# Kernel tuning notes

Measured on AMD Instinct MI355X. Metric: run time of the kernel, lower is better.

The kernel has to match this reference:

```python
import jax, jax.numpy as jnp
import numpy as np

# dims
N, E, Z, C, NB = 8192, 131072, 10, 128, 8
R_MAX, P_CUT, AVG_NEIGH = 5.0, 5, 16.0
SH_DIM, N_L, N_LAYERS, MLP_H = 16, 4, 2, 16
# which l each of the 16 sh components belongs to
L_OF_M = jnp.array([0, 1, 1, 1, 2, 2, 2, 2, 2, 3, 3, 3, 3, 3, 3, 3])


def spherical_harmonics(u):
    """Real spherical harmonics up to l=3, e3nn 'component' normalization. u: [E,3] unit vectors."""
    x, y, z = u[:, 0], u[:, 1], u[:, 2]
    x2, y2, z2 = x * x, y * y, z * z
    s3, s5, s15 = np.sqrt(3.0), np.sqrt(5.0), np.sqrt(15.0)
    a33, a32, a31, a30 = 0.25 * np.sqrt(70.0), np.sqrt(105.0), 0.25 * np.sqrt(42.0), 0.5 * np.sqrt(7.0)
    Y = [jnp.ones_like(x),
         s3 * x, s3 * y, s3 * z,
         s15 * x * y, s15 * y * z, 0.5 * s5 * (3 * z2 - 1.0), s15 * x * z, 0.5 * s15 * (x2 - y2),
         a33 * y * (3 * x2 - y2), a32 * x * y * z, a31 * y * (5 * z2 - 1.0),
         a30 * z * (5 * z2 - 3.0), a31 * x * (5 * z2 - 1.0), 0.5 * a32 * z * (x2 - y2),
         a33 * x * (x2 - 3 * y2)]
    return jnp.stack(Y, axis=-1)  # [E,16]


def radial_embedding(r):
    """Bessel radial basis with smooth polynomial cutoff (p=5). r: [E] edge lengths."""
    x = r / R_MAX
    p = float(P_CUT)
    cut = (1.0 - 0.5 * (p + 1.0) * (p + 2.0) * x ** P_CUT
           + p * (p + 2.0) * x ** (P_CUT + 1) - 0.5 * p * (p + 1.0) * x ** (P_CUT + 2))
    cut = jnp.where(x < 1.0, cut, 0.0)
    n = jnp.arange(1, NB + 1, dtype=r.dtype)
    bessel = np.sqrt(2.0 / R_MAX) * jnp.sin(n[None, :] * jnp.pi * x[:, None]) / r[:, None]
    return bessel * cut[:, None]  # [E,8]


def _forward(positions, node_attrs, shifts, W_embed, W_up, R_w1, R_w2, R_w3,
             W_out, w_sc, w_prod, W_plin, w_ro0, ro_w1, ro_w2, edge_index):
    sender, receiver = edge_index[0], edge_index[1]
    vec = positions[receiver] - positions[sender] + shifts          # [E,3]
    lengths = jnp.linalg.norm(vec, axis=-1) + 1e-9                  # [E]
    sh = spherical_harmonics(vec / lengths[:, None])                # [E,16]
    edge_feats = radial_embedding(lengths)                          # [E,8]

    # node embedding: scalars into l=0 slot of [N,C,16]
    scalars = node_attrs @ W_embed                                  # [N,C]
    feats = jnp.zeros((N, C, SH_DIM), scalars.dtype).at[:, :, 0].set(scalars)

    outputs = []
    for L in range(N_LAYERS):
        # linear up (channel mixing, per irrep component)
        h = jnp.einsum('ncm,cd->ndm', feats, W_up[L])               # [N,C,16]
        # radial MLP -> per-edge, per-channel, per-l tensor-product weights
        r = jax.nn.silu(edge_feats @ R_w1[L])
        r = jax.nn.silu(r @ R_w2[L])
        w = (r @ R_w3[L]).reshape(E, C, N_L)                        # [E,C,4]
        w_m = jnp.take(w, L_OF_M, axis=2)                           # [E,C,16]
        # channel-wise tensor product: scalar node feat x SH, scatter to receiver
        msg = h[sender, :, 0][:, :, None] * w_m * sh[:, None, :]    # [E,C,16]
        agg = jax.ops.segment_sum(msg, receiver, num_segments=N) / AVG_NEIGH
        m = jnp.einsum('ncm,cd->ndm', agg, W_out[L])                # [N,C,16]
        # element-dependent skip connection
        sc = h * (node_attrs @ w_sc[L])[:, :, None]
        # product basis (correlation 3): element-weighted powers of scalar part
        s = m[:, :, 0]                                              # [N,C]
        coeff = jnp.einsum('nz,zck->nck', node_attrs, w_prod[L])    # [N,C,3]
        powers = jnp.stack([jnp.ones_like(s), s, s * s], axis=-1)   # [N,C,3]
        scale = jnp.sum(coeff * powers, axis=-1)                    # [N,C]
        feats = jnp.einsum('ncm,cd->ndm', m * scale[:, :, None], W_plin[L]) + sc
        if L == 0:
            outputs.append(feats[:, :, 0] @ w_ro0)                  # linear readout [N]
        else:
            outputs.append(jax.nn.silu(feats[:, :, 0] @ ro_w1) @ ro_w2)  # nonlinear readout [N]
    return outputs[0] + outputs[1]


def setup_inputs() -> dict:
    key = jax.random.key(0)
    ks = jax.random.split(key, 16)
    positions = jax.random.normal(ks[0], (N, 3), jnp.float32) * 1.5
    elems = jax.random.randint(ks[1], (N,), 0, Z)
    node_attrs = jax.nn.one_hot(elems, Z, dtype=jnp.float32)
    edge_index = jax.random.randint(ks[2], (2, E), 0, N)
    shifts = jnp.zeros((E, 3), jnp.float32)
    g = lambda k, sh, fan: jax.random.normal(k, sh, jnp.float32) / np.sqrt(fan)
    return {
        'positions': positions, 'node_attrs': node_attrs, 'shifts': shifts,
        'W_embed': g(ks[3], (Z, C), Z),
        'W_up': g(ks[4], (N_LAYERS, C, C), C),
        'R_w1': g(ks[5], (N_LAYERS, NB, 64), NB),
        'R_w2': g(ks[6], (N_LAYERS, 64, 64), 64),
        'R_w3': g(ks[7], (N_LAYERS, 64, C * N_L), 64),
        'W_out': g(ks[8], (N_LAYERS, C, C), C),
        'w_sc': g(ks[9], (N_LAYERS, Z, C), 1),
        'w_prod': g(ks[10], (N_LAYERS, Z, C, 3), 1) * 0.1,
        'W_plin': g(ks[11], (N_LAYERS, C, C), C),
        'w_ro0': g(ks[12], (C,), C),
        'ro_w1': g(ks[13], (C, MLP_H), C),
        'ro_w2': g(ks[14], (MLP_H,), MLP_H),
        'edge_index': edge_index,
    }


def reference(positions, node_attrs, shifts, W_embed, W_up, R_w1, R_w2, R_w3,
              W_out, w_sc, w_prod, W_plin, w_ro0, ro_w1, ro_w2, edge_index):
    return _forward(positions, node_attrs, shifts, W_embed, W_up, R_w1, R_w2, R_w3,
                    W_out, w_sc, w_prod, W_plin, w_ro0, ro_w1, ro_w2, edge_index)
```

## Files before the change

kernel.cpp:

```cpp
#include <hip/hip_runtime.h>
#include <math.h>

constexpr int kN = 8192;
constexpr int kE = 131072;
constexpr int kHalfN = 4096;
constexpr int kWbTiles = 544;
constexpr int kWbRows  = kWbTiles * 128;

typedef short bf16x8 __attribute__((ext_vector_type(8)));
typedef float f32x4 __attribute__((ext_vector_type(4)));
typedef unsigned short ushort_t;
typedef unsigned int uint_t;

__device__ __forceinline__ float silu_f(float x) { return x / (1.f + __expf(-x)); }

__device__ __forceinline__ ushort_t f2b(float f) {
  uint_t x = __float_as_uint(f);
  uint_t r = (x + 0x7fffu + ((x >> 16) & 1u)) >> 16;
  return (ushort_t)r;
}
__device__ __forceinline__ float b2f(ushort_t u) {
  return __uint_as_float(((uint_t)u) << 16);
}

__global__ __launch_bounds__(256) void zero_ints_kernel(int* __restrict__ a, int* __restrict__ b) {
  int i = blockIdx.x * 256 + threadIdx.x;
  if (i < kN) { a[i] = 0; b[i] = 0; }
}

__global__ __launch_bounds__(256) void elem_kernel(const float* __restrict__ attrs, int* __restrict__ elem) {
  int n = blockIdx.x * 256 + threadIdx.x;
  if (n >= kN) return;
  const float* a = attrs + (size_t)n * 10;
  int best = 0; float bv = a[0];
  #pragma unroll
  for (int z = 1; z < 10; ++z) { float v = a[z]; if (v > bv) { bv = v; best = z; } }
  elem[n] = best;
}

__global__ __launch_bounds__(256) void init_feats_kernel(const float* __restrict__ W_embed,
                                                         const int* __restrict__ elem,
                                                         ushort_t* __restrict__ F) {
  int i = blockIdx.x * 256 + threadIdx.x;
  int n = i >> 7, c = i & 127;
  F[(size_t)n * 2048 + c] = f2b(W_embed[(size_t)elem[n] * 128 + c]);
}

__global__ __launch_bounds__(256) void geom_kernel(const float* __restrict__ pos,
                                                   const float* __restrict__ shifts,
                                                   const int* __restrict__ ei,
                                                   float* __restrict__ sh,
                                                   float* __restrict__ rb) {
  int e = blockIdx.x * 256 + threadIdx.x;
  if (e >= kE) return;
  int s = ei[e], r = ei[kE + e];
  float vx = pos[r*3+0] - pos[s*3+0] + shifts[(size_t)e*3+0];
  float vy = pos[r*3+1] - pos[s*3+1] + shifts[(size_t)e*3+1];
  float vz = pos[r*3+2] - pos[s*3+2] + shifts[(size_t)e*3+2];
  float len = sqrtf(vx*vx + vy*vy + vz*vz) + 1e-9f;
  float inv = 1.f / len;
  float x = vx*inv, y = vy*inv, z = vz*inv;
  float x2 = x*x, y2 = y*y, z2 = z*z;
  const float s3  = 1.7320508075688772f;
  const float s5  = 2.2360679774997896f;
  const float s15 = 3.8729833462074170f;
  const float a33 = 2.0916500663351889f;
  const float a32 = 10.246950765959598f;
  const float a31 = 1.6201851746019651f;
  const float a30 = 1.3228756555322954f;
  float4* shp = (float4*)(sh + (size_t)e * 16);
  shp[0] = make_float4(1.f, s3*x, s3*y, s3*z);
  shp[1] = make_float4(s15*x*y, s15*y*z, 0.5f*s5*(3.f*z2 - 1.f), s15*x*z);
  shp[2] = make_float4(0.5f*s15*(x2 - y2), a33*y*(3.f*x2 - y2), a32*x*y*z, a31*y*(5.f*z2 - 1.f));
  shp[3] = make_float4(a30*z*(5.f*z2 - 3.f), a31*x*(5.f*z2 - 1.f), 0.5f*a32*z*(x2 - y2), a33*x*(x2 - 3.f*y2));
  float xr = len * 0.2f;
  float cut = 0.f;
  if (xr < 1.f) {
    float x5 = xr*xr*xr*xr*xr;
    cut = 1.f - 21.f*x5 + 35.f*x5*xr - 15.f*x5*xr*xr;
  }
  float pref = 0.63245553203367587f * cut * inv;
  const float PI = 3.14159265358979323846f;
  float theta = PI * xr;
  float sn, cs;
  __sincosf(theta, &sn, &cs);
  float twoc = 2.f * cs;
  float b[8];
  float s_prev = 0.f, s_cur = sn;
  b[0] = pref * s_cur;
  #pragma unroll
  for (int k = 1; k < 8; ++k) {
    float s_next = twoc * s_cur - s_prev;
    s_prev = s_cur; s_cur = s_next;
    b[k] = pref * s_cur;
  }
  float4* rbp = (float4*)(rb + (size_t)e * 8);
  rbp[0] = make_float4(b[0], b[1], b[2], b[3]);
  rbp[1] = make_float4(b[4], b[5], b[6], b[7]);
}

__global__ __launch_bounds__(256) void count_kernel(const int* __restrict__ ei, int* __restrict__ counts) {
  int e = blockIdx.x * 256 + threadIdx.x;
  if (e < kE) atomicAdd(&counts[ei[kE + e]], 1);
}

__global__ __launch_bounds__(1024) void scan_kernel(const int* __restrict__ counts, int* __restrict__ offs) {
  __shared__ int tmp[1024];
  int t = threadIdx.x;
  int loc[8]; int s = 0;
  #pragma unroll
  for (int i = 0; i < 8; ++i) { loc[i] = s; s += counts[t*8 + i]; }
  tmp[t] = s;
  __syncthreads();
  for (int d = 1; d < 1024; d <<= 1) {
    int v = (t >= d) ? tmp[t - d] : 0;
    __syncthreads();
    tmp[t] += v;
    __syncthreads();
  }
  int pre = (t == 0) ? 0 : tmp[t - 1];
  #pragma unroll
  for (int i = 0; i < 8; ++i) offs[t*8 + i] = pre + loc[i];
  if (t == 1023) offs[kN] = tmp[1023];
}

__global__ __launch_bounds__(256) void fill_kernel(const int* __restrict__ ei, const int* __restrict__ offs,
                                                   int* __restrict__ cursor, int* __restrict__ eids) {
  int e = blockIdx.x * 256 + threadIdx.x;
  if (e >= kE) return;
  int r = ei[kE + e];
  int pos = atomicAdd(&cursor[r], 1);
  eids[offs[r] + pos] = e;
}

__global__ __launch_bounds__(256) void radial_kernel(const float* __restrict__ rb,
                                                     const float* __restrict__ W1,
                                                     const float* __restrict__ W2,
                                                     ushort_t* __restrict__ r2) {
  __shared__ float rbs[128][8];
  __shared__ float W1s[8*64];
  __shared__ ushort_t B2s[64][72];
  __shared__ ushort_t r1s[128][72];
  const int tid = threadIdx.x;
  const size_t ebase = (size_t)blockIdx.x * 128;
  {
    int r = tid >> 1, q = tid & 1;
    *(float4*)&rbs[r][q*4] = *(const float4*)&rb[(ebase + r)*8 + q*4];
  }
  for (int i = tid; i < 512; i += 256) W1s[i] = W1[i];
  for (int i = tid; i < 4096; i += 256) {
    int k = i >> 6, col = i & 63;
    B2s[col][k] = f2b(W2[i]);
  }
  __syncthreads();
  {
    int col = tid & 63;
    int r0 = (tid >> 6) * 32;
    #pragma unroll 4
    for (int rr = 0; rr < 32; ++rr) {
      int row = r0 + rr;
      float v = 0.f;
      #pragma unroll
      for (int i = 0; i < 8; ++i) v = fmaf(rbs[row][i], W1s[i*64 + col], v);
      r1s[row][col] = f2b(silu_f(v));
    }
  }
  __syncthreads();
  const int lane = tid & 63, wv = tid >> 6;
  const int wr = wv * 32;
  const int fr = lane & 15, kg = (lane >> 4) * 8;
  f32x4 acc[2][4] = {};
  #pragma unroll
  for (int ks = 0; ks < 2; ++ks) {
    const int k0 = ks*32 + kg;
    bf16x8 af[2], bfr[4];
    #pragma unroll
    for (int i = 0; i < 2; ++i) af[i] = *(const bf16x8*)&r1s[wr + i*16 + fr][k0];
    #pragma unroll
    for (int j = 0; j < 4; ++j) bfr[j] = *(const bf16x8*)&B2s[j*16 + fr][k0];
    #pragma unroll
    for (int i = 0; i < 2; ++i)
      #pragma unroll
      for (int j = 0; j < 4; ++j)
        acc[i][j] = __builtin_amdgcn_mfma_f32_16x16x32_bf16(af[i], bfr[j], acc[i][j], 0, 0, 0);
  }
  __syncthreads();
  const int dcol = lane & 15, drow4 = (lane >> 4) * 4;
  #pragma unroll
  for (int i = 0; i < 2; ++i)
    #pragma unroll
    for (int j = 0; j < 4; ++j)
      #pragma unroll
      for (int r = 0; r < 4; ++r) {
        int row = wr + i*16 + drow4 + r;
        int col = j*16 + dcol;
        r1s[row][col] = f2b(silu_f(acc[i][j][r]));
      }
  __syncthreads();
  for (int idx = tid * 8; idx < 128*64; idx += 256*8) {
    int r = idx >> 6, k = idx & 63;
    *(int4*)&r2[(ebase + r)*64 + k] = *(const int4*)&r1s[r][k];
  }
}

__global__ __launch_bounds__(256) void transpose_w_kernel(const float* __restrict__ W, ushort_t* __restrict__ WT) {
  int i = blockIdx.x * 256 + threadIdx.x;
  int d = i >> 7, c = i & 127;
  WT[i] = f2b(W[c*128 + d]);
}

__global__ __launch_bounds__(256) void transpose_r3_kernel(const float* __restrict__ R3, ushort_t* __restrict__ R3T) {
  int i = blockIdx.x * 256 + threadIdx.x;
  int t = i >> 6, j = i & 63;
  R3T[i] = f2b(R3[j*512 + t]);
}

template<bool SCALED, bool EPI, bool L0>
__global__ __launch_bounds__(256) void mgemm_kernel(
    const ushort_t* __restrict__ A, size_t aStride,
    const ushort_t* __restrict__ BT,
    ushort_t* __restrict__ O, size_t oStride,
    const float* __restrict__ scaleBuf,
    const ushort_t* __restrict__ Hbuf,
    const float* __restrict__ wscL,
    const int* __restrict__ elem)
{
  __shared__ ushort_t As[128][136];
  __shared__ ushort_t Bs[128][136];
  const int tid = threadIdx.x;
  const size_t rowbase = (size_t)blockIdx.x * 128;

  for (int idx = tid * 8; idx < 128 * 128; idx += 256 * 8) {
    int r = idx >> 7, k = idx & 127;
    *(int4*)&Bs[r][k] = *(const int4*)&BT[(size_t)r * 128 + k];
  }
  for (int idx = tid * 8; idx < 128 * 128; idx += 256 * 8) {
    int r = idx >> 7, k = idx & 127;
    size_t grow = rowbase + r;
    const ushort_t* ap = A + grow * aStride + k;
    if (SCALED) {
      const float* sp = scaleBuf + (grow >> 4) * 128 + k;
      uint_t u[4];
      #pragma unroll
      for (int q = 0; q < 4; ++q) {
        ushort_t lo = f2b(b2f(ap[2*q])   * sp[2*q]);
        ushort_t hi = f2b(b2f(ap[2*q+1]) * sp[2*q+1]);
        u[q] = (uint_t)lo | ((uint_t)hi << 16);
      }
      *(int4*)&As[r][k] = make_int4((int)u[0], (int)u[1], (int)u[2], (int)u[3]);
    } else {
      *(int4*)&As[r][k] = *(const int4*)ap;
    }
  }
  __syncthreads();

  const int lane = tid & 63, wv = tid >> 6;
  const int wr = (wv >> 1) * 64, wc = (wv & 1) * 64;
  const int fr = lane & 15;
  const int kg = (lane >> 4) * 8;
  f32x4 acc[4][4] = {};
  #pragma unroll
  for (int ks = 0; ks < 4; ++ks) {
    const int k0 = ks * 32 + kg;
    bf16x8 af[4], bfr[4];
    #pragma unroll
    for (int i = 0; i < 4; ++i) af[i]  = *(const bf16x8*)&As[wr + i*16 + fr][k0];
    #pragma unroll
    for (int j = 0; j < 4; ++j) bfr[j] = *(const bf16x8*)&Bs[wc + j*16 + fr][k0];
    #pragma unroll
    for (int i = 0; i < 4; ++i)
      #pragma unroll
      for (int j = 0; j < 4; ++j)
        acc[i][j] = __builtin_amdgcn_mfma_f32_16x16x32_bf16(af[i], bfr[j], acc[i][j], 0, 0, 0);
  }

  const int dcol = lane & 15, drow4 = (lane >> 4) * 4;
  #pragma unroll
  for (int i = 0; i < 4; ++i) {
    #pragma unroll
    for (int j = 0; j < 4; ++j) {
      int col = wc + j*16 + dcol;
      #pragma unroll
      for (int r = 0; r < 4; ++r) {
        int row = wr + i*16 + drow4 + r;
        size_t grow = rowbase + row;
        float v = acc[i][j][r];
        if (EPI) {
          if (!L0 || ((grow & 15) == 0)) {
            int ee = elem[grow >> 4];
            v += b2f(Hbuf[grow * 128 + col]) * wscL[(size_t)ee * 128 + col];
          }
        }
        O[grow * oStride + col] = f2b(v);
      }
    }
  }
}

__global__ __launch_bounds__(256) void wgemm_kernel(
    const ushort_t* __restrict__ r2, const int* __restrict__ eids,
    const int* __restrict__ offs, int nb0,
    const ushort_t* __restrict__ R3T, ushort_t* __restrict__ wb)
{
  __shared__ ushort_t As[128][72];
  __shared__ ushort_t Bs[128][72];
  const int tid = threadIdx.x;
  const int rowbase = blockIdx.x * 128;
  const int colbase = blockIdx.y * 128;
  const int halfStart = offs[nb0];
  const int halfEnd   = offs[nb0 + kHalfN];

  for (int idx = tid * 8; idx < 128 * 64; idx += 256 * 8) {
    int r = idx >> 6, k = idx & 63;
    *(int4*)&Bs[r][k] = *(const int4*)&R3T[(size_t)(colbase + r) * 64 + k];
  }
  for (int idx = tid * 8; idx < 128 * 64; idx += 256 * 8) {
    int r = idx >> 6, k = idx & 63;
    int ii = halfStart + rowbase + r;
    int iic = ii < halfEnd ? ii : (halfEnd - 1);
    if (iic < 0) iic = 0;
    int e = eids[iic];
    *(int4*)&As[r][k] = *(const int4*)&r2[(size_t)e * 64 + k];
  }
  __syncthreads();

  const int lane = tid & 63, wv = tid >> 6;
  const int wr = (wv >> 1) * 64, wc = (wv & 1) * 64;
  const int fr = lane & 15;
  const int kg = (lane >> 4) * 8;
  f32x4 acc[4][4] = {};
  #pragma unroll
  for (int ks = 0; ks < 2; ++ks) {
    const int k0 = ks * 32 + kg;
    bf16x8 af[4], bfr[4];
    #pragma unroll
    for (int i = 0; i < 4; ++i) af[i]  = *(const bf16x8*)&As[wr + i*16 + fr][k0];
    #pragma unroll
    for (int j = 0; j < 4; ++j) bfr[j] = *(const bf16x8*)&Bs[wc + j*16 + fr][k0];
    #pragma unroll
    for (int i = 0; i < 4; ++i)
      #pragma unroll
      for (int j = 0; j < 4; ++j)
        acc[i][j] = __builtin_amdgcn_mfma_f32_16x16x32_bf16(af[i], bfr[j], acc[i][j], 0, 0, 0);
  }

  const int dcol = lane & 15, drow4 = (lane >> 4) * 4;
  #pragma unroll
  for (int i = 0; i < 4; ++i) {
    #pragma unroll
    for (int j = 0; j < 4; ++j) {
      int col = colbase + wc + j*16 + dcol;
      #pragma unroll
      for (int r = 0; r < 4; ++r) {
        int row = rowbase + wr + i*16 + drow4 + r;
        wb[(size_t)row * 512 + col] = f2b(acc[i][j][r]);
      }
    }
  }
}

constexpr int CH = 16;
__global__ __launch_bounds__(512) void gather_kernel(
    const int* __restrict__ offs, const int* __restrict__ eids,
    const int* __restrict__ ei, int nb0,
    const ushort_t* __restrict__ wb,
    const float* __restrict__ sh,
    const ushort_t* __restrict__ H,
    ushort_t* __restrict__ AGG)
{
  __shared__ ushort_t ws[CH][512];
  __shared__ ushort_t h0s[CH][128];
  __shared__ float shs[CH][16];
  int n = nb0 + blockIdx.x;
  int t = threadIdx.x;
  int l = t >> 7;
  int c = t & 127;
  const int wstart = offs[nb0];
  float a0=0,a1=0,a2=0,a3=0,a4=0,a5=0,a6=0;
  const int e0 = offs[n], e1 = offs[n+1];
  for (int base = e0; base < e1; base += CH) {
    const int cnt = min(CH, e1 - base);
    #pragma unroll
    for (int rep = 0; rep < 2; ++rep) {
      int idx = rep * 512 + t;
      int j = idx >> 6, seg = idx & 63;
      if (j < cnt)
        *(int4*)&ws[j][seg * 8] = *(const int4*)&wb[(size_t)(base - wstart + j) * 512 + seg * 8];
    }
    if (t < 256) {
      int j = t >> 4, seg = t & 15;
      if (j < cnt) {
        int e = eids[base + j];
        *(int4*)&h0s[j][seg * 8] = *(const int4*)&H[(size_t)ei[e] * 2048 + seg * 8];
      }
    } else if (t < 320) {
      int tt = t - 256, j = tt >> 2, seg = tt & 3;
      if (j < cnt)
        *(float4*)&shs[j][seg * 4] = *(const float4*)&sh[(size_t)eids[base + j] * 16 + seg * 4];
    }
    __syncthreads();
    for (int j = 0; j < cnt; ++j) {
      float wv = b2f(ws[j][(c << 2) | l]);
      float wh = wv * b2f(h0s[j][c]);
      if (l == 0) {
        a0 = fmaf(wh, shs[j][0], a0);
      } else if (l == 1) {
        float4 s4 = *(const float4*)&shs[j][0];
        a0 = fmaf(wh, s4.y, a0); a1 = fmaf(wh, s4.z, a1); a2 = fmaf(wh, s4.w, a2);
      } else if (l == 2) {
        float4 s4 = *(const float4*)&shs[j][4];
        float s8 = shs[j][8];
        a0 = fmaf(wh, s4.x, a0); a1 = fmaf(wh, s4.y, a1); a2 = fmaf(wh, s4.z, a2);
        a3 = fmaf(wh, s4.w, a3); a4 = fmaf(wh, s8, a4);
      } else {
        float4 sA = *(const float4*)&shs[j][8];
        float4 sB = *(const float4*)&shs[j][12];
        a0 = fmaf(wh, sA.y, a0); a1 = fmaf(wh, sA.z, a1); a2 = fmaf(wh, sA.w, a2);
        a3 = fmaf(wh, sB.x, a3); a4 = fmaf(wh, sB.y, a4); a5 = fmaf(wh, sB.z, a5);
        a6 = fmaf(wh, sB.w, a6);
      }
    }
    __syncthreads();
  }
  const float inv16 = 0.0625f;
  size_t baseo = (size_t)n * 2048 + c;
  if (l == 0) {
    AGG[baseo] = f2b(a0 * inv16);
  } else if (l == 1) {
    AGG[baseo + 1*128] = f2b(a0*inv16); AGG[baseo + 2*128] = f2b(a1*inv16); AGG[baseo + 3*128] = f2b(a2*inv16);
  } else if (l == 2) {
    AGG[baseo + 4*128] = f2b(a0*inv16); AGG[baseo + 5*128] = f2b(a1*inv16); AGG[baseo + 6*128] = f2b(a2*inv16);
    AGG[baseo + 7*128] = f2b(a3*inv16); AGG[baseo + 8*128] = f2b(a4*inv16);
  } else {
    AGG[baseo + 9*128]  = f2b(a0*inv16); AGG[baseo + 10*128] = f2b(a1*inv16); AGG[baseo + 11*128] = f2b(a2*inv16);
    AGG[baseo + 12*128] = f2b(a3*inv16); AGG[baseo + 13*128] = f2b(a4*inv16); AGG[baseo + 14*128] = f2b(a5*inv16);
    AGG[baseo + 15*128] = f2b(a6*inv16);
  }
}

__global__ __launch_bounds__(256) void scale_kernel(const ushort_t* __restrict__ M,
                                                    const int* __restrict__ elem,
                                                    const float* __restrict__ wprodL,
                                                    float* __restrict__ scale) {
  int i = blockIdx.x * 256 + threadIdx.x;
  int n = i >> 7, c = i & 127;
  float s = b2f(M[(size_t)n * 2048 + c]);
  const float* co = wprodL + ((size_t)elem[n] * 128 + c) * 3;
  scale[i] = co[0] + s * (co[1] + s * co[2]);
}

__global__ __launch_bounds__(64) void readout_kernel(const ushort_t* __restrict__ F,
                                                     const float* __restrict__ ro0,
                                                     const float* __restrict__ ro1,
                                                     const float* __restrict__ ro2,
                                                     float* __restrict__ out, int layer) {
  int n = blockIdx.x; int t = threadIdx.x;
  const ushort_t* fr = F + (size_t)n * 2048;
  float f0 = b2f(fr[t]), f1 = b2f(fr[t + 64]);
  if (layer == 0) {
    float v = f0 * ro0[t] + f1 * ro0[t + 64];
    #pragma unroll
    for (int m = 32; m > 0; m >>= 1) v += __shfl_xor(v, m, 64);
    if (t == 0) out[n] = v;
  } else {
    float acc = 0.f;
    for (int h = 0; h < 16; ++h) {
      float p = f0 * ro1[t*16 + h] + f1 * ro1[(t + 64)*16 + h];
      #pragma unroll
      for (int m = 32; m > 0; m >>= 1) p += __shfl_xor(p, m, 64);
      acc = fmaf(silu_f(p), ro2[h], acc);
    }
    if (t == 0) out[n] += acc;
  }
}

extern "C" void kernel_launch(void* const* d_in, const int* in_sizes, int n_in,
                              void* d_out, int out_size, void* d_ws, size_t ws_size,
                              hipStream_t stream) {
  (void)in_sizes; (void)n_in; (void)out_size;
  const float* positions = (const float*)d_in[0];
  const float* node_attrs= (const float*)d_in[1];
  const float* shifts    = (const float*)d_in[2];
  const float* W_embed   = (const float*)d_in[3];
  const float* W_up      = (const float*)d_in[4];
  const float* R_w1      = (const float*)d_in[5];
  const float* R_w2      = (const float*)d_in[6];
  const float* R_w3      = (const float*)d_in[7];
  const float* W_out     = (const float*)d_in[8];
  const float* w_sc      = (const float*)d_in[9];
  const float* w_prod    = (const float*)d_in[10];
  const float* W_plin    = (const float*)d_in[11];
  const float* w_ro0     = (const float*)d_in[12];
  const float* ro_w1     = (const float*)d_in[13];
  const float* ro_w2     = (const float*)d_in[14];
  const int*   ei        = (const int*)d_in[15];
  float* out = (float*)d_out;

  char* ws_ptr = (char*)d_ws;
  size_t off = 0;
  auto alloc = [&](size_t nbytes) -> void* {
    void* p = ws_ptr + off;
    off += (nbytes + 255) & ~(size_t)255;
    return p;
  };
  const size_t PB = (size_t)kN * 16 * 128 * sizeof(ushort_t);
  ushort_t* P0   = (ushort_t*)alloc(PB);
  ushort_t* P1   = (ushort_t*)alloc(PB);
  ushort_t* P2   = (ushort_t*)alloc(PB);
  float* shb     = (float*)alloc((size_t)kE * 16 * 4);
  float* rbb     = (float*)alloc((size_t)kE * 8 * 4);
  ushort_t* r2b  = (ushort_t*)alloc((size_t)kE * 64 * 2);
  float* scaleb  = (float*)alloc((size_t)kN * 128 * 4);
  ushort_t* wb   = (ushort_t*)alloc((size_t)kWbRows * 512 * 2);
  ushort_t* R3T0 = (ushort_t*)alloc(512 * 64 * 2);
  ushort_t* R3T1 = (ushort_t*)alloc(512 * 64 * 2);
  ushort_t* WTu0 = (ushort_t*)alloc(128 * 128 * 2);
  ushort_t* WTu1 = (ushort_t*)alloc(128 * 128 * 2);
  ushort_t* WTo0 = (ushort_t*)alloc(128 * 128 * 2);
  ushort_t* WTo1 = (ushort_t*)alloc(128 * 128 * 2);
  ushort_t* WTp0 = (ushort_t*)alloc(128 * 128 * 2);
  ushort_t* WTp1 = (ushort_t*)alloc(128 * 128 * 2);
  int* elemb  = (int*)alloc(kN * 4);
  int* counts = (int*)alloc(kN * 4);
  int* cursor = (int*)alloc(kN * 4);
  int* offsb  = (int*)alloc((kN + 1) * 4);
  int* eidsb  = (int*)alloc((size_t)kE * 4);
  if (off > ws_size) return;

  zero_ints_kernel<<<kN/256, 256, 0, stream>>>(counts, cursor);
  elem_kernel<<<kN/256, 256, 0, stream>>>(node_attrs, elemb);
  init_feats_kernel<<<(kN*128)/256, 256, 0, stream>>>(W_embed, elemb, P0);
  geom_kernel<<<kE/256, 256, 0, stream>>>(positions, shifts, ei, shb, rbb);
  count_kernel<<<kE/256, 256, 0, stream>>>(ei, counts);
  scan_kernel<<<1, 1024, 0, stream>>>(counts, offsb);
  fill_kernel<<<kE/256, 256, 0, stream>>>(ei, offsb, cursor, eidsb);
  transpose_w_kernel<<<64, 256, 0, stream>>>(W_up, WTu0);
  transpose_w_kernel<<<64, 256, 0, stream>>>(W_up + 16384, WTu1);
  transpose_w_kernel<<<64, 256, 0, stream>>>(W_out, WTo0);
  transpose_w_kernel<<<64, 256, 0, stream>>>(W_out + 16384, WTo1);
  transpose_w_kernel<<<64, 256, 0, stream>>>(W_plin, WTp0);
  transpose_w_kernel<<<64, 256, 0, stream>>>(W_plin + 16384, WTp1);
  transpose_r3_kernel<<<128, 256, 0, stream>>>(R_w3, R3T0);
  transpose_r3_kernel<<<128, 256, 0, stream>>>(R_w3 + 32768, R3T1);

  radial_kernel<<<kE/128, 256, 0, stream>>>(rbb, R_w1, R_w2, r2b);
  mgemm_kernel<false,false,false><<<kN/128, 256, 0, stream>>>(
      P0, 2048, WTu0, P1, 2048, nullptr, nullptr, nullptr, nullptr);
  wgemm_kernel<<<dim3(kWbTiles,4), 256, 0, stream>>>(r2b, eidsb, offsb, 0, R3T0, wb);
  gather_kernel<<<kHalfN, 512, 0, stream>>>(offsb, eidsb, ei, 0, wb, shb, P1, P2);
  wgemm_kernel<<<dim3(kWbTiles,4), 256, 0, stream>>>(r2b, eidsb, offsb, kHalfN, R3T0, wb);
  gather_kernel<<<kHalfN, 512, 0, stream>>>(offsb, eidsb, ei, kHalfN, wb, shb, P1, P2);
  mgemm_kernel<false,false,false><<<(kN*16)/128, 256, 0, stream>>>(
      P2, 128, WTo0, P0, 128, nullptr, nullptr, nullptr, nullptr);
  scale_kernel<<<(kN*128)/256, 256, 0, stream>>>(P0, elemb, w_prod, scaleb);
  mgemm_kernel<true,true,true><<<(kN*16)/128, 256, 0, stream>>>(
      P0, 128, WTp0, P2, 128, scaleb, P1, w_sc, elemb);
  readout_kernel<<<kN, 64, 0, stream>>>(P2, w_ro0, ro_w1, ro_w2, out, 0);

  radial_kernel<<<kE/128, 256, 0, stream>>>(rbb, R_w1 + 512, R_w2 + 4096, r2b);
  mgemm_kernel<false,false,false><<<(kN*16)/128, 256, 0, stream>>>(
      P2, 128, WTu1, P1, 128, nullptr, nullptr, nullptr, nullptr);
  wgemm_kernel<<<dim3(kWbTiles,4), 256, 0, stream>>>(r2b, eidsb, offsb, 0, R3T1, wb);
  gather_kernel<<<kHalfN, 512, 0, stream>>>(offsb, eidsb, ei, 0, wb, shb, P1, P0);
  wgemm_kernel<<<dim3(kWbTiles,4), 256, 0, stream>>>(r2b, eidsb, offsb, kHalfN, R3T1, wb);
  gather_kernel<<<kHalfN, 512, 0, stream>>>(offsb, eidsb, ei, kHalfN, wb, shb, P1, P0);
  mgemm_kernel<false,false,false><<<(kN*16)/128, 256, 0, stream>>>(
      P0, 128, WTo1, P2, 128, nullptr, nullptr, nullptr, nullptr);
  scale_kernel<<<(kN*128)/256, 256, 0, stream>>>(P2, elemb, w_prod + 3840, scaleb);
  mgemm_kernel<true,true,false><<<(kN*16)/128, 256, 0, stream>>>(
      P2, 128, WTp1, P0, 128, scaleb, P1, w_sc + 1280, elemb);
  readout_kernel<<<kN, 64, 0, stream>>>(P0, w_ro0, ro_w1, ro_w2, out, 1);
}
```

Baseline: 471.1 us.

## Fuse per-edge R3 weight GEMM into gather and store edge data in CSR order

Measured after the change: 662.1 us. 40.5% more time.

```diff
diff --git a/kernel.cpp b/kernel.cpp
--- a/kernel.cpp
+++ b/kernel.cpp
@@ -3,9 +3,6 @@
 
 constexpr int kN = 8192;
 constexpr int kE = 131072;
-constexpr int kHalfN = 4096;
-constexpr int kWbTiles = 544;
-constexpr int kWbRows  = kWbTiles * 128;
 
 typedef short bf16x8 __attribute__((ext_vector_type(8)));
 typedef float f32x4 __attribute__((ext_vector_type(4)));
@@ -46,14 +43,55 @@
   F[(size_t)n * 2048 + c] = f2b(W_embed[(size_t)elem[n] * 128 + c]);
 }
 
+__global__ __launch_bounds__(256) void count_kernel(const int* __restrict__ ei, int* __restrict__ counts) {
+  int e = blockIdx.x * 256 + threadIdx.x;
+  if (e < kE) atomicAdd(&counts[ei[kE + e]], 1);
+}
+
+__global__ __launch_bounds__(1024) void scan_kernel(const int* __restrict__ counts, int* __restrict__ offs) {
+  __shared__ int tmp[1024];
+  int t = threadIdx.x;
+  int loc[8]; int s = 0;
+  #pragma unroll
+  for (int i = 0; i < 8; ++i) { loc[i] = s; s += counts[t*8 + i]; }
+  tmp[t] = s;
+  __syncthreads();
+  for (int d = 1; d < 1024; d <<= 1) {
+    int v = (t >= d) ? tmp[t - d] : 0;
+    __syncthreads();
+    tmp[t] += v;
+    __syncthreads();
+  }
+  int pre = (t == 0) ? 0 : tmp[t - 1];
+  #pragma unroll
+  for (int i = 0; i < 8; ++i) offs[t*8 + i] = pre + loc[i];
+  if (t == 1023) offs[kN] = tmp[1023];
+}
+
+__global__ __launch_bounds__(256) void fill_kernel(const int* __restrict__ ei, const int* __restrict__ offs,
+                                                   int* __restrict__ cursor, int* __restrict__ eids,
+                                                   int* __restrict__ sends) {
+  int e = blockIdx.x * 256 + threadIdx.x;
+  if (e >= kE) return;
+  int s = ei[e];
+  int r = ei[kE + e];
+  int pos = atomicAdd(&cursor[r], 1);
+  eids[offs[r] + pos] = e;
+  sends[offs[r] + pos] = s;
+}
+
 __global__ __launch_bounds__(256) void geom_kernel(const float* __restrict__ pos,
                                                    const float* __restrict__ shifts,
                                                    const int* __restrict__ ei,
+                                                   const int* __restrict__ eids,
+                                                   const int* __restrict__ sends,
                                                    float* __restrict__ sh,
                                                    float* __restrict__ rb) {
-  int e = blockIdx.x * 256 + threadIdx.x;
-  if (e >= kE) return;
-  int s = ei[e], r = ei[kE + e];
+  int slot = blockIdx.x * 256 + threadIdx.x;
+  if (slot >= kE) return;
+  int e = eids[slot];
+  int s = sends[slot];
+  int r = ei[kE + e];
   float vx = pos[r*3+0] - pos[s*3+0] + shifts[(size_t)e*3+0];
   float vy = pos[r*3+1] - pos[s*3+1] + shifts[(size_t)e*3+1];
   float vz = pos[r*3+2] - pos[s*3+2] + shifts[(size_t)e*3+2];
@@ -68,7 +106,7 @@
   const float a32 = 10.246950765959598f;
   const float a31 = 1.6201851746019651f;
   const float a30 = 1.3228756555322954f;
-  float4* shp = (float4*)(sh + (size_t)e * 16);
+  float4* shp = (float4*)(sh + (size_t)slot * 16);
   shp[0] = make_float4(1.f, s3*x, s3*y, s3*z);
   shp[1] = make_float4(s15*x*y, s15*y*z, 0.5f*s5*(3.f*z2 - 1.f), s15*x*z);
   shp[2] = make_float4(0.5f*s15*(x2 - y2), a33*y*(3.f*x2 - y2), a32*x*y*z, a31*y*(5.f*z2 - 1.f));
@@ -94,43 +132,9 @@
     s_prev = s_cur; s_cur = s_next;
     b[k] = pref * s_cur;
   }
-  float4* rbp = (float4*)(rb + (size_t)e * 8);
+  float4* rbp = (float4*)(rb + (size_t)slot * 8);
   rbp[0] = make_float4(b[0], b[1], b[2], b[3]);
   rbp[1] = make_float4(b[4], b[5], b[6], b[7]);
-}
-
-__global__ __launch_bounds__(256) void count_kernel(const int* __restrict__ ei, int* __restrict__ counts) {
-  int e = blockIdx.x * 256 + threadIdx.x;
-  if (e < kE) atomicAdd(&counts[ei[kE + e]], 1);
-}
-
-__global__ __launch_bounds__(1024) void scan_kernel(const int* __restrict__ counts, int* __restrict__ offs) {
-  __shared__ int tmp[1024];
-  int t = threadIdx.x;
-  int loc[8]; int s = 0;
-  #pragma unroll
-  for (int i = 0; i < 8; ++i) { loc[i] = s; s += counts[t*8 + i]; }
-  tmp[t] = s;
-  __syncthreads();
-  for (int d = 1; d < 1024; d <<= 1) {
-    int v = (t >= d) ? tmp[t - d] : 0;
-    __syncthreads();
-    tmp[t] += v;
-    __syncthreads();
-  }
-  int pre = (t == 0) ? 0 : tmp[t - 1];
-  #pragma unroll
-  for (int i = 0; i < 8; ++i) offs[t*8 + i] = pre + loc[i];
-  if (t == 1023) offs[kN] = tmp[1023];
-}
-
-__global__ __launch_bounds__(256) void fill_kernel(const int* __restrict__ ei, const int* __restrict__ offs,
-                                                   int* __restrict__ cursor, int* __restrict__ eids) {
-  int e = blockIdx.x * 256 + threadIdx.x;
-  if (e >= kE) return;
-  int r = ei[kE + e];
-  int pos = atomicAdd(&cursor[r], 1);
-  eids[offs[r] + pos] = e;
 }
 
 __global__ __launch_bounds__(256) void radial_kernel(const float* __restrict__ rb,
@@ -212,7 +216,8 @@
 __global__ __launch_bounds__(256) void transpose_r3_kernel(const float* __restrict__ R3, ushort_t* __restrict__ R3T) {
   int i = blockIdx.x * 256 + threadIdx.x;
   int t = i >> 6, j = i & 63;
-  R3T[i] = f2b(R3[j*512 + t]);
+  int c = t & 127, l = t >> 7;
+  R3T[i] = f2b(R3[j*512 + c*4 + l]);
 }
 
 template<bool SCALED, bool EPI, bool L0>
@@ -297,144 +302,92 @@
   }
 }
 
-__global__ __launch_bounds__(256) void wgemm_kernel(
-    const ushort_t* __restrict__ r2, const int* __restrict__ eids,
-    const int* __restrict__ offs, int nb0,
-    const ushort_t* __restrict__ R3T, ushort_t* __restrict__ wb)
-{
-  __shared__ ushort_t As[128][72];
-  __shared__ ushort_t Bs[128][72];
-  const int tid = threadIdx.x;
-  const int rowbase = blockIdx.x * 128;
-  const int colbase = blockIdx.y * 128;
-  const int halfStart = offs[nb0];
-  const int halfEnd   = offs[nb0 + kHalfN];
-
-  for (int idx = tid * 8; idx < 128 * 64; idx += 256 * 8) {
-    int r = idx >> 6, k = idx & 63;
-    *(int4*)&Bs[r][k] = *(const int4*)&R3T[(size_t)(colbase + r) * 64 + k];
-  }
-  for (int idx = tid * 8; idx < 128 * 64; idx += 256 * 8) {
-    int r = idx >> 6, k = idx & 63;
-    int ii = halfStart + rowbase + r;
-    int iic = ii < halfEnd ? ii : (halfEnd - 1);
-    if (iic < 0) iic = 0;
-    int e = eids[iic];
-    *(int4*)&As[r][k] = *(const int4*)&r2[(size_t)e * 64 + k];
-  }
-  __syncthreads();
-
-  const int lane = tid & 63, wv = tid >> 6;
-  const int wr = (wv >> 1) * 64, wc = (wv & 1) * 64;
-  const int fr = lane & 15;
-  const int kg = (lane >> 4) * 8;
-  f32x4 acc[4][4] = {};
-  #pragma unroll
-  for (int ks = 0; ks < 2; ++ks) {
-    const int k0 = ks * 32 + kg;
-    bf16x8 af[4], bfr[4];
-    #pragma unroll
-    for (int i = 0; i < 4; ++i) af[i]  = *(const bf16x8*)&As[wr + i*16 + fr][k0];
-    #pragma unroll
-    for (int j = 0; j < 4; ++j) bfr[j] = *(const bf16x8*)&Bs[wc + j*16 + fr][k0];
-    #pragma unroll
-    for (int i = 0; i < 4; ++i)
-      #pragma unroll
-      for (int j = 0; j < 4; ++j)
-        acc[i][j] = __builtin_amdgcn_mfma_f32_16x16x32_bf16(af[i], bfr[j], acc[i][j], 0, 0, 0);
-  }
-
-  const int dcol = lane & 15, drow4 = (lane >> 4) * 4;
-  #pragma unroll
-  for (int i = 0; i < 4; ++i) {
-    #pragma unroll
-    for (int j = 0; j < 4; ++j) {
-      int col = colbase + wc + j*16 + dcol;
-      #pragma unroll
-      for (int r = 0; r < 4; ++r) {
-        int row = rowbase + wr + i*16 + drow4 + r;
-        wb[(size_t)row * 512 + col] = f2b(acc[i][j][r]);
-      }
-    }
-  }
-}
-
-constexpr int CH = 16;
 __global__ __launch_bounds__(512) void gather_kernel(
-    const int* __restrict__ offs, const int* __restrict__ eids,
-    const int* __restrict__ ei, int nb0,
-    const ushort_t* __restrict__ wb,
-    const float* __restrict__ sh,
+    const int* __restrict__ offs, const int* __restrict__ sends,
+    const ushort_t* __restrict__ r2csr,
+    const float* __restrict__ shcsr,
+    const ushort_t* __restrict__ R3T,
     const ushort_t* __restrict__ H,
     ushort_t* __restrict__ AGG)
 {
-  __shared__ ushort_t ws[CH][512];
-  __shared__ ushort_t h0s[CH][128];
-  __shared__ float shs[CH][16];
-  int n = nb0 + blockIdx.x;
-  int t = threadIdx.x;
-  int l = t >> 7;
-  int c = t & 127;
-  const int wstart = offs[nb0];
-  float a0=0,a1=0,a2=0,a3=0,a4=0,a5=0,a6=0;
+  __shared__ ushort_t r2s[16][72];
+  __shared__ ushort_t h0s[16][140];
+  __shared__ float shs[16][16];
+  const int n = blockIdx.x;
+  const int tid = threadIdx.x;
+  const int lane = tid & 63, wid = tid >> 6;
+  const int l = wid >> 1;
+  const int cb = (wid & 1) * 64;
+  const int fr = lane & 15, kg = (lane >> 4) * 8;
+
+  bf16x8 bfrag[4][2];
+  #pragma unroll
+  for (int j = 0; j < 4; ++j)
+    #pragma unroll
+    for (int ks = 0; ks < 2; ++ks)
+      bfrag[j][ks] = *(const bf16x8*)&R3T[(size_t)(wid*64 + j*16 + fr)*64 + ks*32 + kg];
+
+  float agg[7][4] = {};
   const int e0 = offs[n], e1 = offs[n+1];
-  for (int base = e0; base < e1; base += CH) {
-    const int cnt = min(CH, e1 - base);
-    #pragma unroll
-    for (int rep = 0; rep < 2; ++rep) {
-      int idx = rep * 512 + t;
-      int j = idx >> 6, seg = idx & 63;
-      if (j < cnt)
-        *(int4*)&ws[j][seg * 8] = *(const int4*)&wb[(size_t)(base - wstart + j) * 512 + seg * 8];
-    }
-    if (t < 256) {
-      int j = t >> 4, seg = t & 15;
-      if (j < cnt) {
-        int e = eids[base + j];
-        *(int4*)&h0s[j][seg * 8] = *(const int4*)&H[(size_t)ei[e] * 2048 + seg * 8];
+  for (int base = e0; base < e1; base += 16) {
+    const int cnt = min(16, e1 - base);
+    if (tid < 128) {
+      int row = tid >> 3, seg = tid & 7;
+      int4 v = make_int4(0,0,0,0);
+      if (row < cnt) v = *(const int4*)&r2csr[(size_t)(base + row)*64 + seg*8];
+      *(int4*)&r2s[row][seg*8] = v;
+    } else if (tid < 384) {
+      int x = tid - 128;
+      int row = x >> 4, seg = x & 15;
+      int4 v = make_int4(0,0,0,0);
+      if (row < cnt) v = *(const int4*)&H[(size_t)sends[base + row]*2048 + seg*8];
+      *(int4*)&h0s[row][seg*8] = v;
+    } else if (tid < 448) {
+      int x = tid - 384;
+      int row = x >> 2, seg = x & 3;
+      float4 v = make_float4(0.f,0.f,0.f,0.f);
+      if (row < cnt) v = *(const float4*)&shcsr[(size_t)(base + row)*16 + seg*4];
+      *(float4*)&shs[row][seg*4] = v;
+    }
+    __syncthreads();
+    bf16x8 af0 = *(const bf16x8*)&r2s[fr][kg];
+    bf16x8 af1 = *(const bf16x8*)&r2s[fr][32 + kg];
+    f32x4 wacc[4];
+    #pragma unroll
+    for (int j = 0; j < 4; ++j) {
+      f32x4 a = {};
+      a = __builtin_amdgcn_mfma_f32_16x16x32_bf16(af0, bfrag[j][0], a, 0, 0, 0);
+      a = __builtin_amdgcn_mfma_f32_16x16x32_bf16(af1, bfrag[j][1], a, 0, 0, 0);
+      wacc[j] = a;
+    }
+    #pragma unroll
+    for (int j = 0; j < 4; ++j) {
+      #pragma unroll
+      for (int r = 0; r < 4; ++r) {
+        int e = (lane >> 4) * 4 + r;
+        float wh = wacc[j][r] * b2f(h0s[e][cb + j*16 + fr]);
+        #pragma unroll
+        for (int mi = 0; mi < 7; ++mi) {
+          if (mi <= 2*l)
+            agg[mi][j] = fmaf(wh, shs[e][l*l + mi], agg[mi][j]);
+        }
       }
-    } else if (t < 320) {
-      int tt = t - 256, j = tt >> 2, seg = tt & 3;
-      if (j < cnt)
-        *(float4*)&shs[j][seg * 4] = *(const float4*)&sh[(size_t)eids[base + j] * 16 + seg * 4];
     }
     __syncthreads();
-    for (int j = 0; j < cnt; ++j) {
-      float wv = b2f(ws[j][(c << 2) | l]);
-      float wh = wv * b2f(h0s[j][c]);
-      if (l == 0) {
-        a0 = fmaf(wh, shs[j][0], a0);
-      } else if (l == 1) {
-        float4 s4 = *(const float4*)&shs[j][0];
-        a0 = fmaf(wh, s4.y, a0); a1 = fmaf(wh, s4.z, a1); a2 = fmaf(wh, s4.w, a2);
-      } else if (l == 2) {
-        float4 s4 = *(const float4*)&shs[j][4];
-        float s8 = shs[j][8];
-        a0 = fmaf(wh, s4.x, a0); a1 = fmaf(wh, s4.y, a1); a2 = fmaf(wh, s4.z, a2);
-        a3 = fmaf(wh, s4.w, a3); a4 = fmaf(wh, s8, a4);
-      } else {
-        float4 sA = *(const float4*)&shs[j][8];
-        float4 sB = *(const float4*)&shs[j][12];
-        a0 = fmaf(wh, sA.y, a0); a1 = fmaf(wh, sA.z, a1); a2 = fmaf(wh, sA.w, a2);
-        a3 = fmaf(wh, sB.x, a3); a4 = fmaf(wh, sB.y, a4); a5 = fmaf(wh, sB.z, a5);
-        a6 = fmaf(wh, sB.w, a6);
+  }
+  const float inv16 = 0.0625f;
+  #pragma unroll
+  for (int mi = 0; mi < 7; ++mi) {
+    if (mi <= 2*l) {
+      #pragma unroll
+      for (int j = 0; j < 4; ++j) {
+        float v = agg[mi][j];
+        v += __shfl_xor(v, 16, 64);
+        v += __shfl_xor(v, 32, 64);
+        if (lane < 16)
+          AGG[(size_t)n*2048 + (l*l + mi)*128 + cb + j*16 + lane] = f2b(v * inv16);
       }
     }
-    __syncthreads();
-  }
-  const float inv16 = 0.0625f;
-  size_t baseo = (size_t)n * 2048 + c;
-  if (l == 0) {
-    AGG[baseo] = f2b(a0 * inv16);
-  } else if (l == 1) {
-    AGG[baseo + 1*128] = f2b(a0*inv16); AGG[baseo + 2*128] = f2b(a1*inv16); AGG[baseo + 3*128] = f2b(a2*inv16);
-  } else if (l == 2) {
-    AGG[baseo + 4*128] = f2b(a0*inv16); AGG[baseo + 5*128] = f2b(a1*inv16); AGG[baseo + 6*128] = f2b(a2*inv16);
-    AGG[baseo + 7*128] = f2b(a3*inv16); AGG[baseo + 8*128] = f2b(a4*inv16);
-  } else {
-    AGG[baseo + 9*128]  = f2b(a0*inv16); AGG[baseo + 10*128] = f2b(a1*inv16); AGG[baseo + 11*128] = f2b(a2*inv16);
-    AGG[baseo + 12*128] = f2b(a3*inv16); AGG[baseo + 13*128] = f2b(a4*inv16); AGG[baseo + 14*128] = f2b(a5*inv16);
-    AGG[baseo + 15*128] = f2b(a6*inv16);
   }
 }
 
@@ -504,36 +457,36 @@
     return p;
   };
   const size_t PB = (size_t)kN * 16 * 128 * sizeof(ushort_t);
-  ushort_t* P0   = (ushort_t*)alloc(PB);
-  ushort_t* P1   = (ushort_t*)alloc(PB);
-  ushort_t* P2   = (ushort_t*)alloc(PB);
-  float* shb     = (float*)alloc((size_t)kE * 16 * 4);
-  float* rbb     = (float*)alloc((size_t)kE * 8 * 4);
-  ushort_t* r2b  = (ushort_t*)alloc((size_t)kE * 64 * 2);
-  float* scaleb  = (float*)alloc((size_t)kN * 128 * 4);
-  ushort_t* wb   = (ushort_t*)alloc((size_t)kWbRows * 512 * 2);
-  ushort_t* R3T0 = (ushort_t*)alloc(512 * 64 * 2);
-  ushort_t* R3T1 = (ushort_t*)alloc(512 * 64 * 2);
-  ushort_t* WTu0 = (ushort_t*)alloc(128 * 128 * 2);
-  ushort_t* WTu1 = (ushort_t*)alloc(128 * 128 * 2);
-  ushort_t* WTo0 = (ushort_t*)alloc(128 * 128 * 2);
-  ushort_t* WTo1 = (ushort_t*)alloc(128 * 128 * 2);
-  ushort_t* WTp0 = (ushort_t*)alloc(128 * 128 * 2);
-  ushort_t* WTp1 = (ushort_t*)alloc(128 * 128 * 2);
+  ushort_t* P0    = (ushort_t*)alloc(PB);
+  ushort_t* P1    = (ushort_t*)alloc(PB);
+  ushort_t* P2    = (ushort_t*)alloc(PB);
+  float* shcsr    = (float*)alloc((size_t)kE * 16 * 4);
+  float* rbcsr    = (float*)alloc((size_t)kE * 8 * 4);
+  ushort_t* r2csr = (ushort_t*)alloc((size_t)kE * 64 * 2);
+  float* scaleb   = (float*)alloc((size_t)kN * 128 * 4);
+  ushort_t* R3T0  = (ushort_t*)alloc(512 * 64 * 2);
+  ushort_t* R3T1  = (ushort_t*)alloc(512 * 64 * 2);
+  ushort_t* WTu0  = (ushort_t*)alloc(128 * 128 * 2);
+  ushort_t* WTu1  = (ushort_t*)alloc(128 * 128 * 2);
+  ushort_t* WTo0  = (ushort_t*)alloc(128 * 128 * 2);
+  ushort_t* WTo1  = (ushort_t*)alloc(128 * 128 * 2);
+  ushort_t* WTp0  = (ushort_t*)alloc(128 * 128 * 2);
+  ushort_t* WTp1  = (ushort_t*)alloc(128 * 128 * 2);
   int* elemb  = (int*)alloc(kN * 4);
   int* counts = (int*)alloc(kN * 4);
   int* cursor = (int*)alloc(kN * 4);
   int* offsb  = (int*)alloc((kN + 1) * 4);
   int* eidsb  = (int*)alloc((size_t)kE * 4);
+  int* sendsb = (int*)alloc((size_t)kE * 4);
   if (off > ws_size) return;
 
   zero_ints_kernel<<<kN/256, 256, 0, stream>>>(counts, cursor);
   elem_kernel<<<kN/256, 256, 0, stream>>>(node_attrs, elemb);
   init_feats_kernel<<<(kN*128)/256, 256, 0, stream>>>(W_embed, elemb, P0);
-  geom_kernel<<<kE/256, 256, 0, stream>>>(positions, shifts, ei, shb, rbb);
   count_kernel<<<kE/256, 256, 0, stream>>>(ei, counts);
   scan_kernel<<<1, 1024, 0, stream>>>(counts, offsb);
-  fill_kernel<<<kE/256, 256, 0, stream>>>(ei, offsb, cursor, eidsb);
+  fill_kernel<<<kE/256, 256, 0, stream>>>(ei, offsb, cursor, eidsb, sendsb);
+  geom_kernel<<<kE/256, 256, 0, stream>>>(positions, shifts, ei, eidsb, sendsb, shcsr, rbcsr);
   transpose_w_kernel<<<64, 256, 0, stream>>>(W_up, WTu0);
   transpose_w_kernel<<<64, 256, 0, stream>>>(W_up + 16384, WTu1);
   transpose_w_kernel<<<64, 256, 0, stream>>>(W_out, WTo0);
@@ -543,13 +496,10 @@
   transpose_r3_kernel<<<128, 256, 0, stream>>>(R_w3, R3T0);
   transpose_r3_kernel<<<128, 256, 0, stream>>>(R_w3 + 32768, R3T1);
 
-  radial_kernel<<<kE/128, 256, 0, stream>>>(rbb, R_w1, R_w2, r2b);
+  radial_kernel<<<kE/128, 256, 0, stream>>>(rbcsr, R_w1, R_w2, r2csr);
   mgemm_kernel<false,false,false><<<kN/128, 256, 0, stream>>>(
       P0, 2048, WTu0, P1, 2048, nullptr, nullptr, nullptr, nullptr);
-  wgemm_kernel<<<dim3(kWbTiles,4), 256, 0, stream>>>(r2b, eidsb, offsb, 0, R3T0, wb);
-  gather_kernel<<<kHalfN, 512, 0, stream>>>(offsb, eidsb, ei, 0, wb, shb, P1, P2);
-  wgemm_kernel<<<dim3(kWbTiles,4), 256, 0, stream>>>(r2b, eidsb, offsb, kHalfN, R3T0, wb);
-  gather_kernel<<<kHalfN, 512, 0, stream>>>(offsb, eidsb, ei, kHalfN, wb, shb, P1, P2);
+  gather_kernel<<<kN, 512, 0, stream>>>(offsb, sendsb, r2csr, shcsr, R3T0, P1, P2);
   mgemm_kernel<false,false,false><<<(kN*16)/128, 256, 0, stream>>>(
       P2, 128, WTo0, P0, 128, nullptr, nullptr, nullptr, nullptr);
   scale_kernel<<<(kN*128)/256, 256, 0, stream>>>(P0, elemb, w_prod, scaleb);
@@ -557,13 +507,10 @@
       P0, 128, WTp0, P2, 128, scaleb, P1, w_sc, elemb);
   readout_kernel<<<kN, 64, 0, stream>>>(P2, w_ro0, ro_w1, ro_w2, out, 0);
 
-  radial_kernel<<<kE/128, 256, 0, stream>>>(rbb, R_w1 + 512, R_w2 + 4096, r2b);
+  radial_kernel<<<kE/128, 256, 0, stream>>>(rbcsr, R_w1 + 512, R_w2 + 4096, r2csr);
   mgemm_kernel<false,false,false><<<(kN*16)/128, 256, 0, stream>>>(
       P2, 128, WTu1, P1, 128, nullptr, nullptr, nullptr, nullptr);
-  wgemm_kernel<<<dim3(kWbTiles,4), 256, 0, stream>>>(r2b, eidsb, offsb, 0, R3T1, wb);
-  gather_kernel<<<kHalfN, 512, 0, stream>>>(offsb, eidsb, ei, 0, wb, shb, P1, P0);
-  wgemm_kernel<<<dim3(kWbTiles,4), 256, 0, stream>>>(r2b, eidsb, offsb, kHalfN, R3T1, wb);
-  gather_kernel<<<kHalfN, 512, 0, stream>>>(offsb, eidsb, ei, kHalfN, wb, shb, P1, P0);
+  gather_kernel<<<kN, 512, 0, stream>>>(offsb, sendsb, r2csr, shcsr, R3T1, P1, P0);
   mgemm_kernel<false,false,false><<<(kN*16)/128, 256, 0, stream>>>(
       P0, 128, WTo1, P2, 128, nullptr, nullptr, nullptr, nullptr);
   scale_kernel<<<(kN*128)/256, 256, 0, stream>>>(P2, elemb, w_prod + 3840, scaleb);
```
